# Kernel optimization log

Measured on AMD Instinct MI355X. Metric: run time of the kernel, lower is better.

Reference implementation:

```python
import jax, jax.numpy as jnp
import numpy as np

K = 6
EPS = 1e-7
BN_EPS = 1e-5


def tagconv(x, row, col, n, lins, bias, mw1, mb1, bng, bnb, mw2, mb2):
    # gcn_norm: symmetric normalization, no self-loops, edge_weight = 1
    deg = jax.ops.segment_sum(jnp.ones(row.shape[0], x.dtype), col, num_segments=n)
    dis = jnp.where(deg > 0, jax.lax.rsqrt(jnp.maximum(deg, 1.0)), 0.0)
    norm = dis[row] * dis[col]  # [E]
    out = x @ lins[0]
    h = x
    for k in range(1, K + 1):
        # message: relu(edge_weight * x_j) + eps, then scatter-add to destination
        msg = jax.nn.relu(norm[:, None] * h[row]) + EPS  # [E, C]
        h = jax.ops.segment_sum(msg, col, num_segments=n)
        out = out + h @ lins[k]
    out = out + bias
    # MLP: Linear -> BatchNorm1d(eval: running mean 0, var 1) -> ReLU -> Dropout(eval) -> Linear
    z = out @ mw1 + mb1
    z = bng * (z * (1.0 / np.sqrt(1.0 + BN_EPS))) + bnb
    z = jax.nn.relu(z)
    return z @ mw2 + mb2


def setup_inputs() -> dict:
    key = jax.random.key(0)
    ks = jax.random.split(key, 8)
    N, E, F, H, C = 50000, 800000, 128, 128, 64
    s = 0.05
    return {
        "x": jax.random.normal(ks[0], (N, F), jnp.float32),
        "edge_index": jax.random.randint(ks[1], (2, E), 0, N, jnp.int64),
        "lins1": jax.random.normal(ks[2], (K + 1, F, H), jnp.float32) * s,
        "bias1": jnp.zeros((H,), jnp.float32),
        "m1w1": jax.random.normal(ks[3], (H, 2 * H), jnp.float32) * s,
        "m1b1": jnp.zeros((2 * H,), jnp.float32),
        "bn1g": jnp.ones((2 * H,), jnp.float32),
        "bn1b": jnp.zeros((2 * H,), jnp.float32),
        "m1w2": jax.random.normal(ks[4], (2 * H, H), jnp.float32) * s,
        "m1b2": jnp.zeros((H,), jnp.float32),
        "lins2": jax.random.normal(ks[5], (K + 1, H, C), jnp.float32) * s,
        "bias2": jnp.zeros((C,), jnp.float32),
        "m2w1": jax.random.normal(ks[6], (C, 2 * C), jnp.float32) * s,
        "m2b1": jnp.zeros((2 * C,), jnp.float32),
        "bn2g": jnp.ones((2 * C,), jnp.float32),
        "bn2b": jnp.zeros((2 * C,), jnp.float32),
        "m2w2": jax.random.normal(ks[7], (2 * C, C), jnp.float32) * s,
        "m2b2": jnp.zeros((C,), jnp.float32),
    }


def reference(x, edge_index, lins1, bias1, m1w1, m1b1, bn1g, bn1b, m1w2, m1b2,
              lins2, bias2, m2w1, m2b1, bn2g, bn2b, m2w2, m2b2):
    n = x.shape[0]
    row, col = edge_index[0], edge_index[1]
    h = tagconv(x, row, col, n, lins1, bias1, m1w1, m1b1, bn1g, bn1b, m1w2, m1b2)
    h = jax.nn.relu(h)  # dropout is identity in eval mode
    return tagconv(h, row, col, n, lins2, bias2, m2w1, m2b1, bn2g, bn2b, m2w2, m2b2)
```

## Files before the change

### kernel.cpp

```cpp
#include <hip/hip_runtime.h>
#include <hip/hip_bf16.h>


#define EPS_MSG 1e-7f
#define BNSCALE 0.9999950000374997f
#define LO_INV 0.0009765625f

typedef _Float16 half_t;
typedef _Float16 f16x8 __attribute__((ext_vector_type(8)));
typedef float f32x4 __attribute__((ext_vector_type(4)));

__device__ __forceinline__ void gld16(const char* g, char* l) {
    __builtin_amdgcn_global_load_lds(
        (const __attribute__((address_space(1))) void*)g,
        (__attribute__((address_space(3))) void*)l, 16, 0, 0);
}

__device__ __forceinline__ float hlo(unsigned p) {
    unsigned short u = (unsigned short)(p & 0xffffu);
    half_t h;
    __builtin_memcpy(&h, &u, 2);
    return (float)h;
}
__device__ __forceinline__ float hhi(unsigned p) {
    unsigned short u = (unsigned short)(p >> 16);
    half_t h;
    __builtin_memcpy(&h, &u, 2);
    return (float)h;
}
__device__ __forceinline__ unsigned fpack2(float x, float y) {
    half_t a = (half_t)x, b = (half_t)y;
    unsigned short ua, ub;
    __builtin_memcpy(&ua, &a, 2);
    __builtin_memcpy(&ub, &b, 2);
    return (unsigned)ua | ((unsigned)ub << 16);
}


__global__ void zero_i32(int* __restrict__ p, int n) {
    int i = blockIdx.x * blockDim.x + threadIdx.x;
    if (i < n) p[i] = 0;
}

__global__ void count_deg(const int* __restrict__ col, int* __restrict__ deg, int E) {
    int e = blockIdx.x * blockDim.x + threadIdx.x;
    if (e < E) atomicAdd(&deg[col[e]], 1);
}

__global__ void compute_dis_s(const int* __restrict__ deg, float* __restrict__ dis,
                              float* __restrict__ s, float* __restrict__ rs, int N) {
    int v = blockIdx.x * blockDim.x + threadIdx.x;
    if (v >= N) return;
    int d = deg[v];
    float di = (d > 0) ? rsqrtf((float)d) : 0.f;
    dis[v] = di;
    s[v] = (d > 0) ? di : 1.f;
    rs[v] = (d > 0) ? sqrtf((float)d) : 1.f;
}

__global__ void scan_blk(const int* __restrict__ deg, int* __restrict__ off,
                         int* __restrict__ bsum, int N) {
    __shared__ int sm[1024];
    int i = blockIdx.x * 1024 + threadIdx.x;
    sm[threadIdx.x] = (i < N) ? deg[i] : 0;
    __syncthreads();
    for (int ofs = 1; ofs < 1024; ofs <<= 1) {
        int t = (threadIdx.x >= (unsigned)ofs) ? sm[threadIdx.x - ofs] : 0;
        __syncthreads();
        sm[threadIdx.x] += t;
        __syncthreads();
    }
    if (i < N) off[i + 1] = sm[threadIdx.x];
    if (threadIdx.x == 0) bsum[blockIdx.x] = sm[1023];
}

__global__ void scan_top(int* __restrict__ bsum, int nb) {
    if (threadIdx.x == 0 && blockIdx.x == 0) {
        int a = 0;
        for (int b = 0; b < nb; ++b) {
            int t = bsum[b];
            bsum[b] = a;
            a += t;
        }
    }
}

__global__ void scan_add(int* __restrict__ off, const int* __restrict__ bsum, int N) {
    int i = blockIdx.x * 1024 + threadIdx.x;
    if (i < N) off[i + 1] += bsum[blockIdx.x];
    if (i == 0) off[0] = 0;
}

__global__ void fill_edges(const int* __restrict__ row, const int* __restrict__ col,
                           const int* __restrict__ off, int* __restrict__ cur,
                           unsigned short* __restrict__ esrc, int E) {
    int e = blockIdx.x * blockDim.x + threadIdx.x;
    if (e >= E) return;
    int c = col[e];
    int pos = off[c] + atomicAdd(&cur[c], 1);
    esrc[pos] = (unsigned short)row[e];
}


__global__ void conv_xg(const float* __restrict__ x, half_t* __restrict__ slab,
                        half_t* __restrict__ g0, const float* __restrict__ dis,
                        const float* __restrict__ s, int total) {
    int i = blockIdx.x * blockDim.x + threadIdx.x;
    if (i >= total) return;
    int v = i >> 7, c = i & 127;
    float xv = x[i];
    slab[(size_t)v * 896 + c] = (half_t)(s[v] * xv);
    g0[i] = (half_t)(dis[v] * fmaxf(xv, 0.f));
}

__device__ __forceinline__ void wcv(const float* __restrict__ in, half_t* __restrict__ oh,
                                    half_t* __restrict__ ol, int nm, int K, int Nn, int i) {
    int KT = nm * K;
    int n = i / KT;
    int rem = i - n * KT;
    int km = rem / K, k = rem - km * K;
    float w = in[(size_t)km * K * Nn + (size_t)k * Nn + n];
    half_t h = (half_t)w;
    oh[i] = h;
    ol[i] = (half_t)((w - (float)h) * 1024.f);
}

__global__ void conv_all(const float* l1, const float* l2, const float* a1, const float* b1,
                         const float* a2, const float* b2, half_t* W1h, half_t* W1l,
                         half_t* W2h, half_t* W2l, half_t* M1ah, half_t* M1al, half_t* M1bh,
                         half_t* M1bl, half_t* M2ah, half_t* M2al, half_t* M2bh,
                         half_t* M2bl) {
    int i = blockIdx.x * blockDim.x + threadIdx.x;
    if (i < 114688) {
        wcv(l1, W1h, W1l, 7, 128, 128, i);
    } else if (i < 172032) {
        int j = i - 114688;
        int np = j >> 7, k = j & 127;
        int km = np >> 6, n = np & 63;
        float w = l2[(size_t)km * 128 * 64 + (size_t)k * 64 + n];
        half_t h = (half_t)w;
        W2h[j] = h;
        W2l[j] = (half_t)((w - (float)h) * 1024.f);
    } else if (i < 204800) {
        wcv(a1, M1ah, M1al, 1, 128, 256, i - 172032);
    } else if (i < 237568) {
        wcv(b1, M1bh, M1bl, 1, 256, 128, i - 204800);
    } else if (i < 245760) {
        wcv(a2, M2ah, M2al, 1, 64, 128, i - 237568);
    } else if (i < 253952) {
        wcv(b2, M2bh, M2bl, 1, 128, 64, i - 245760);
    }
}

__global__ void conv_trows(const float* __restrict__ l2, float* __restrict__ T) {
    __shared__ float sm[256];
    int j = blockIdx.x;
    int c = threadIdx.x & 63;
    int part = threadIdx.x >> 6;
    float a = 0.f;
    for (int k = j + 1; k <= 6; ++k)
        for (int kk = part; kk < 128; kk += 4)
            a += l2[(size_t)k * 128 * 64 + kk * 64 + c];
    sm[threadIdx.x] = a;
    __syncthreads();
    if (part == 0) T[j * 64 + c] = (sm[c] + sm[64 + c]) + (sm[128 + c] + sm[192 + c]);
}


__global__ void __launch_bounds__(256) prop(const unsigned* __restrict__ gin, int idl,
                                            unsigned* __restrict__ gout, int odl,
                                            const float* __restrict__ dis,
                                            const int* __restrict__ off,
                                            const unsigned short* __restrict__ esrc, int N) {
    const int lane = threadIdx.x & 63;
    const int w = threadIdx.x >> 6;
    const int stride = gridDim.x * 4;
    for (int v = blockIdx.x * 4 + w; v < N; v += stride) {
        int s = off[v], e = off[v + 1];
        float2 A0 = {0.f, 0.f}, A1 = {0.f, 0.f}, A2 = {0.f, 0.f}, A3 = {0.f, 0.f};
        float2 A4 = {0.f, 0.f}, A5 = {0.f, 0.f}, A6 = {0.f, 0.f}, A7 = {0.f, 0.f};
        for (int i = s; i < e; i += 8) {
            unsigned p[8];
            int ok[8];
#pragma unroll
            for (int j = 0; j < 8; ++j) {
                int ij = i + j;
                ok[j] = ij < e;
                int idx = ok[j] ? ij : e - 1;
                p[j] = gin[esrc[idx] * idl + lane];
            }
            A0.x += ok[0] ? hlo(p[0]) : 0.f; A0.y += ok[0] ? hhi(p[0]) : 0.f;
            A1.x += ok[1] ? hlo(p[1]) : 0.f; A1.y += ok[1] ? hhi(p[1]) : 0.f;
            A2.x += ok[2] ? hlo(p[2]) : 0.f; A2.y += ok[2] ? hhi(p[2]) : 0.f;
            A3.x += ok[3] ? hlo(p[3]) : 0.f; A3.y += ok[3] ? hhi(p[3]) : 0.f;
            A4.x += ok[4] ? hlo(p[4]) : 0.f; A4.y += ok[4] ? hhi(p[4]) : 0.f;
            A5.x += ok[5] ? hlo(p[5]) : 0.f; A5.y += ok[5] ? hhi(p[5]) : 0.f;
            A6.x += ok[6] ? hlo(p[6]) : 0.f; A6.y += ok[6] ? hhi(p[6]) : 0.f;
            A7.x += ok[7] ? hlo(p[7]) : 0.f; A7.y += ok[7] ? hhi(p[7]) : 0.f;
        }
        float ax = ((A0.x + A1.x) + (A2.x + A3.x)) + ((A4.x + A5.x) + (A6.x + A7.x));
        float ay = ((A0.y + A1.y) + (A2.y + A3.y)) + ((A4.y + A5.y) + (A6.y + A7.y));
        float dv = dis[v];
        float ce = (float)(e - s) * EPS_MSG;
        float hx = fmaf(dv, ax, ce);
        float hy = fmaf(dv, ay, ce);
        gout[v * odl + lane] = fpack2(dv * hx, dv * hy);
    }
}


template <int FINAL>
__global__ void __launch_bounds__(256) prop64(
    const half_t* __restrict__ uin, int ldu, const half_t* __restrict__ pj, int ldp,
    half_t* __restrict__ uout, int ldo, const float* __restrict__ dis,
    const int* __restrict__ off, const unsigned short* __restrict__ esrc,
    const float* __restrict__ tj, const float* __restrict__ bias2, int N) {
    const int c = threadIdx.x & 63;
    const int w = threadIdx.x >> 6;
    const int stride = gridDim.x * 4;
    for (int v = blockIdx.x * 4 + w; v < N; v += stride) {
        int s = off[v], e = off[v + 1];
        float a0 = 0.f, a1 = 0.f, a2 = 0.f, a3 = 0.f;
        float a4 = 0.f, a5 = 0.f, a6 = 0.f, a7 = 0.f;
        for (int i = s; i < e; i += 8) {
            float q[8];
            int ok[8];
#pragma unroll
            for (int j = 0; j < 8; ++j) {
                int ij = i + j;
                ok[j] = ij < e;
                int idx = ok[j] ? ij : e - 1;
                q[j] = (float)uin[(size_t)esrc[idx] * ldu + c];
            }
            a0 += ok[0] ? q[0] : 0.f;
            a1 += ok[1] ? q[1] : 0.f;
            a2 += ok[2] ? q[2] : 0.f;
            a3 += ok[3] ? q[3] : 0.f;
            a4 += ok[4] ? q[4] : 0.f;
            a5 += ok[5] ? q[5] : 0.f;
            a6 += ok[6] ? q[6] : 0.f;
            a7 += ok[7] ? q[7] : 0.f;
        }
        float acc = ((a0 + a1) + (a2 + a3)) + ((a4 + a5) + (a6 + a7));
        float dv = dis[v];
        float base = (float)pj[(size_t)v * ldp + c] + (float)(e - s) * EPS_MSG * tj[c];
        float u = fmaf(dv, acc, base);
        if (FINAL)
            uout[(size_t)v * ldo + c] = (half_t)(u + bias2[c]);
        else
            uout[(size_t)v * ldo + c] = (half_t)(dv * u);
    }
}


template <int OUTF32>
__global__ __launch_bounds__(256) void gemm(
    int M, int kiters, const half_t* __restrict__ A, int lda,
    const half_t* __restrict__ Bhp, const half_t* __restrict__ Blp, int ldb, int noff,
    void* __restrict__ Cp, int ldc, const float* __restrict__ rs, int epi,
    const float* __restrict__ bias, const float* __restrict__ bng,
    const float* __restrict__ bnb) {
    constexpr int BM = 64, BK = 64, BN = 64;
    constexpr int WROWS = 16;
    constexpr int NF = 4;
    constexpr int ABY = BM * BK * 2;
    constexpr int BBY = BN * BK * 2;
    constexpr int BUFBY = ABY + 2 * BBY;
    constexpr int ACW = 2, BCW = 2;

    __shared__ char lds[2][BUFBY];

    const int tid = threadIdx.x;
    const int lane = tid & 63;
    const int w = tid >> 6;
    const int m0 = blockIdx.x * BM;
    const int n0 = blockIdx.y * BN + noff;
    const int l15 = lane & 15, lq = lane >> 4;
    const int lr8 = lane >> 3, lc8 = lane & 7;

    const char* gA = (const char*)A;
    const char* gBh = (const char*)Bhp;
    const char* gBl = (const char*)Blp;
    const size_t ldaB = (size_t)lda * 2, ldbB = (size_t)ldb * 2;

    auto stage = [&](int kt, int buf) {
        const int k0b = kt * BK * 2;
        char* base = lds[0] + buf * BUFBY;
#pragma unroll
        for (int i = 0; i < ACW; ++i) {
            int c = w * ACW + i;
            int r = c * 8 + lr8;
            int gv = m0 + r;
            if (gv >= M) gv = M - 1;
            int sc = (lc8 ^ (r & 7)) << 4;
            gld16(gA + (size_t)gv * ldaB + k0b + sc, base + c * 1024);
        }
#pragma unroll
        for (int i = 0; i < BCW; ++i) {
            int c = w * BCW + i;
            int r = c * 8 + lr8;
            int sc = (lc8 ^ (r & 7)) << 4;
            size_t goff = (size_t)(n0 + r) * ldbB + k0b + sc;
            gld16(gBh + goff, base + ABY + c * 1024);
            gld16(gBl + goff, base + ABY + BBY + c * 1024);
        }
    };

    f32x4 acch[NF], accl[NF];
#pragma unroll
    for (int fn = 0; fn < NF; ++fn) {
        acch[fn] = (f32x4){0.f, 0.f, 0.f, 0.f};
        accl[fn] = (f32x4){0.f, 0.f, 0.f, 0.f};
    }

    auto compute = [&](int buf) {
        const char* Ab = lds[0] + buf * BUFBY;
        const char* Bhb = Ab + ABY;
        const char* Blb = Ab + ABY + BBY;
#pragma unroll
        for (int ks = 0; ks < 2; ++ks) {
            const int cc = ks * 4 + lq;
            int ra = w * WROWS + l15;
            f16x8 af = *(const f16x8*)(Ab + ra * 128 + ((cc ^ (ra & 7)) << 4));
#pragma unroll
            for (int fn = 0; fn < NF; ++fn) {
                int r = fn * 16 + l15;
                int o = r * 128 + ((cc ^ (r & 7)) << 4);
                f16x8 bhv = *(const f16x8*)(Bhb + o);
                f16x8 blv = *(const f16x8*)(Blb + o);
                acch[fn] = __builtin_amdgcn_mfma_f32_16x16x32_f16(af, bhv, acch[fn], 0, 0, 0);
                accl[fn] = __builtin_amdgcn_mfma_f32_16x16x32_f16(af, blv, accl[fn], 0, 0, 0);
            }
        }
    };

    stage(0, 0);
    int buf = 0;
    for (int kt = 0; kt < kiters; ++kt) {
        __syncthreads();
        if (kt + 1 < kiters) stage(kt + 1, buf ^ 1);
        compute(buf);
        buf ^= 1;
    }

#pragma unroll
    for (int fn = 0; fn < NF; ++fn)
#pragma unroll
        for (int i = 0; i < 4; ++i) {
            int gr = m0 + w * WROWS + (lane >> 4) * 4 + i;
            if (gr >= M) continue;
            int gc = n0 + fn * 16 + (lane & 15);
            float v = acch[fn][i] + accl[fn][i] * LO_INV;
            if (rs) v *= rs[gr];
            if (epi == 1) {
                v += bias[gc];
            } else if (epi == 2) {
                v = bng[gc] * ((v + bias[gc]) * BNSCALE) + bnb[gc];
                v = fmaxf(v, 0.f);
            } else if (epi == 3) {
                v = fmaxf(v + bias[gc], 0.f);
            }
            if (OUTF32)
                ((float*)Cp)[(size_t)gr * ldc + gc] = v;
            else
                ((half_t*)Cp)[(size_t)gr * ldc + gc] = (half_t)v;
        }
}

extern "C" void kernel_launch(void* const* d_in, const int* in_sizes, int n_in,
                              void* d_out, int out_size, void* d_ws, size_t ws_size,
                              hipStream_t stream) {
    const float* x     = (const float*)d_in[0];
    const int*   ei    = (const int*)d_in[1];
    const float* lins1 = (const float*)d_in[2];
    const float* bias1 = (const float*)d_in[3];
    const float* m1w1  = (const float*)d_in[4];
    const float* m1b1  = (const float*)d_in[5];
    const float* bn1g  = (const float*)d_in[6];
    const float* bn1b  = (const float*)d_in[7];
    const float* m1w2  = (const float*)d_in[8];
    const float* m1b2  = (const float*)d_in[9];
    const float* lins2 = (const float*)d_in[10];
    const float* bias2 = (const float*)d_in[11];
    const float* m2w1  = (const float*)d_in[12];
    const float* m2b1  = (const float*)d_in[13];
    const float* bn2g  = (const float*)d_in[14];
    const float* bn2b  = (const float*)d_in[15];
    const float* m2w2  = (const float*)d_in[16];
    const float* m2b2  = (const float*)d_in[17];
    float* out = (float*)d_out;

    const int N = in_sizes[0] / 128;
    const int E = in_sizes[1] / 2;
    const int* row = ei;
    const int* col = ei + E;

    char* ws = (char*)d_ws;
    size_t o = 0;
    auto alloc = [&](size_t bytes) {
        void* p = ws + o;
        o += (bytes + 255) & ~(size_t)255;
        return p;
    };
    int*            deg  = (int*)alloc((size_t)N * 4);
    int*            cur  = (int*)alloc((size_t)N * 4);
    float*          dis  = (float*)alloc((size_t)N * 4);
    float*          sA   = (float*)alloc((size_t)N * 4);
    float*          rsA  = (float*)alloc((size_t)N * 4);
    int*            off  = (int*)alloc((size_t)(N + 1) * 4);
    int*            bsum = (int*)alloc(1024 * 4);
    float*          Trow = (float*)alloc(6 * 64 * 4);
    unsigned short* esrc = (unsigned short*)alloc((size_t)E * 2);
    half_t* g0    = (half_t*)alloc((size_t)N * 128 * 2);
    half_t* ACC   = (half_t*)alloc((size_t)N * 128 * 2);
    half_t* Z     = (half_t*)alloc((size_t)N * 256 * 2);
    half_t* H1    = (half_t*)alloc((size_t)N * 128 * 2);
    half_t* ACC2  = (half_t*)alloc((size_t)N * 64 * 2);
    half_t* Wc1h  = (half_t*)alloc((size_t)128 * 896 * 2);
    half_t* Wc1l  = (half_t*)alloc((size_t)128 * 896 * 2);
    half_t* Wc2h  = (half_t*)alloc((size_t)448 * 128 * 2);
    half_t* Wc2l  = (half_t*)alloc((size_t)448 * 128 * 2);
    half_t* Wm1ah = (half_t*)alloc((size_t)256 * 128 * 2);
    half_t* Wm1al = (half_t*)alloc((size_t)256 * 128 * 2);
    half_t* Wm1bh = (half_t*)alloc((size_t)128 * 256 * 2);
    half_t* Wm1bl = (half_t*)alloc((size_t)128 * 256 * 2);
    half_t* Wm2ah = (half_t*)alloc((size_t)128 * 64 * 2);
    half_t* Wm2al = (half_t*)alloc((size_t)128 * 64 * 2);
    half_t* Wm2bh = (half_t*)alloc((size_t)64 * 128 * 2);
    half_t* Wm2bl = (half_t*)alloc((size_t)64 * 128 * 2);
    half_t* slab  = (half_t*)alloc((size_t)N * 896 * 2);
    (void)ws_size;

    const int TPB = 256;
    const int nb = (N + 1023) / 1024;
    zero_i32<<<(N + TPB - 1) / TPB, TPB, 0, stream>>>(deg, N);
    zero_i32<<<(N + TPB - 1) / TPB, TPB, 0, stream>>>(cur, N);
    count_deg<<<(E + TPB - 1) / TPB, TPB, 0, stream>>>(col, deg, E);
    compute_dis_s<<<(N + TPB - 1) / TPB, TPB, 0, stream>>>(deg, dis, sA, rsA, N);
    scan_blk<<<nb, 1024, 0, stream>>>(deg, off, bsum, N);
    scan_top<<<1, 64, 0, stream>>>(bsum, nb);
    scan_add<<<nb, 1024, 0, stream>>>(off, bsum, N);
    fill_edges<<<(E + TPB - 1) / TPB, TPB, 0, stream>>>(row, col, off, cur, esrc, E);
    conv_all<<<(253952 + TPB - 1) / TPB, TPB, 0, stream>>>(
        lins1, lins2, m1w1, m1w2, m2w1, m2w2, Wc1h, Wc1l, Wc2h, Wc2l, Wm1ah, Wm1al, Wm1bh,
        Wm1bl, Wm2ah, Wm2al, Wm2bh, Wm2bl);
    conv_trows<<<6, 256, 0, stream>>>(lins2, Trow);
    conv_xg<<<(N * 128 + TPB - 1) / TPB, TPB, 0, stream>>>(x, slab, g0, dis, sA, N * 128);

    unsigned* slabU = (unsigned*)slab;
    unsigned* g0U = (unsigned*)g0;
    const int HG = (N + 63) / 64;

    prop<<<2048, 256, 0, stream>>>(g0U, 64, slabU + 64, 448, dis, off, esrc, N);
    for (int k = 2; k <= 6; ++k)
        prop<<<2048, 256, 0, stream>>>(slabU + (size_t)(k - 1) * 64, 448,
                                       slabU + (size_t)k * 64, 448, dis, off, esrc, N);
    gemm<0><<<dim3(HG, 2), 256, 0, stream>>>(
        N, 14, slab, 896, Wc1h, Wc1l, 896, 0, ACC, 128, rsA, 1, bias1, nullptr, nullptr);
    gemm<0><<<dim3(HG, 4), 256, 0, stream>>>(
        N, 2, ACC, 128, Wm1ah, Wm1al, 128, 0, Z, 256, nullptr, 2, m1b1, bn1g, bn1b);
    gemm<0><<<dim3(HG, 2), 256, 0, stream>>>(
        N, 4, Z, 256, Wm1bh, Wm1bl, 256, 0, H1, 128, nullptr, 3, m1b2, nullptr, nullptr);

    gemm<0><<<dim3(HG, 6), 256, 0, stream>>>(
        N, 2, H1, 128, Wc2h, Wc2l, 128, 0, slab, 448, nullptr, 0, nullptr, nullptr, nullptr);
    gemm<0><<<dim3(HG, 1), 256, 0, stream>>>(
        N, 2, H1, 128, Wc2h, Wc2l, 128, 384, slab, 448, dis, 0, nullptr, nullptr, nullptr);

    half_t* ub0 = g0;
    half_t* ub1 = g0 + (size_t)N * 64;
    prop64<0><<<2048, 256, 0, stream>>>(slab + 384, 448, slab + 320, 448, ub0, 64, dis, off,
                                        esrc, Trow + 5 * 64, nullptr, N);
    prop64<0><<<2048, 256, 0, stream>>>(ub0, 64, slab + 256, 448, ub1, 64, dis, off, esrc,
                                        Trow + 4 * 64, nullptr, N);
    prop64<0><<<2048, 256, 0, stream>>>(ub1, 64, slab + 192, 448, ub0, 64, dis, off, esrc,
                                        Trow + 3 * 64, nullptr, N);
    prop64<0><<<2048, 256, 0, stream>>>(ub0, 64, slab + 128, 448, ub1, 64, dis, off, esrc,
                                        Trow + 2 * 64, nullptr, N);
    prop64<0><<<2048, 256, 0, stream>>>(ub1, 64, slab + 64, 448, ub0, 64, dis, off, esrc,
                                        Trow + 1 * 64, nullptr, N);
    prop64<1><<<2048, 256, 0, stream>>>(ub0, 64, slab, 448, ACC2, 64, dis, off, esrc,
                                        Trow + 0 * 64, bias2, N);

    gemm<0><<<dim3(HG, 2), 256, 0, stream>>>(
        N, 1, ACC2, 64, Wm2ah, Wm2al, 64, 0, Z, 128, nullptr, 2, m2b1, bn2g, bn2b);
    gemm<1><<<dim3(HG, 1), 256, 0, stream>>>(
        N, 2, Z, 128, Wm2bh, Wm2bl, 128, 0, out, 64, nullptr, 1, m2b2, nullptr, nullptr);
}
```

Before: 722.1 us.

## Load each A row tile once and loop over all output column strips

Replaces the 2D-grid GEMM, which re-read the A tile once per 64-wide column block, with two kernels. gemmc computes the full 128-wide output per block using a 2x2 wave layout with BK=32. gemmn keeps the whole 64xK A tile resident in LDS and streams B strips through it, double-buffered. It also merges the two separate lins2 GEMM launches into one, with a row scale applied to the last strip. The goal is to cut redundant global reads of A and launch count, at the cost of more LDS per block and serialised column strips within a block.

```diff
diff --git a/kernel.cpp b/kernel.cpp
--- a/kernel.cpp
+++ b/kernel.cpp
@@ -34,6 +34,21 @@
     __builtin_memcpy(&ua, &a, 2);
     __builtin_memcpy(&ub, &b, 2);
     return (unsigned)ua | ((unsigned)ub << 16);
+}
+
+__device__ __forceinline__ float epi_apply(float v, int gc, int epi,
+                                           const float* __restrict__ bias,
+                                           const float* __restrict__ bng,
+                                           const float* __restrict__ bnb) {
+    if (epi == 1) {
+        v += bias[gc];
+    } else if (epi == 2) {
+        v = bng[gc] * ((v + bias[gc]) * BNSCALE) + bnb[gc];
+        v = fmaxf(v, 0.f);
+    } else if (epi == 3) {
+        v = fmaxf(v + bias[gc], 0.f);
+    }
+    return v;
 }
 
 
@@ -253,30 +268,19 @@
 }
 
 
-template <int OUTF32>
-__global__ __launch_bounds__(256) void gemm(
+__global__ __launch_bounds__(256) void gemmc(
     int M, int kiters, const half_t* __restrict__ A, int lda,
-    const half_t* __restrict__ Bhp, const half_t* __restrict__ Blp, int ldb, int noff,
-    void* __restrict__ Cp, int ldc, const float* __restrict__ rs, int epi,
-    const float* __restrict__ bias, const float* __restrict__ bng,
-    const float* __restrict__ bnb) {
-    constexpr int BM = 64, BK = 64, BN = 64;
-    constexpr int WROWS = 16;
-    constexpr int NF = 4;
-    constexpr int ABY = BM * BK * 2;
-    constexpr int BBY = BN * BK * 2;
-    constexpr int BUFBY = ABY + 2 * BBY;
-    constexpr int ACW = 2, BCW = 2;
-
-    __shared__ char lds[2][BUFBY];
-
-    const int tid = threadIdx.x;
-    const int lane = tid & 63;
-    const int w = tid >> 6;
-    const int m0 = blockIdx.x * BM;
-    const int n0 = blockIdx.y * BN + noff;
+    const half_t* __restrict__ Bhp, const half_t* __restrict__ Blp, int ldb,
+    half_t* __restrict__ Cp, int ldc, const float* __restrict__ rs,
+    const float* __restrict__ bias) {
+    constexpr int ABY = 4096, BBY = 8192, BUFBY = ABY + 2 * BBY;
+    __shared__ __align__(16) char lds[2][BUFBY];
+
+    const int tid = threadIdx.x, lane = tid & 63, w = tid >> 6;
+    const int wr = w >> 1, wc = w & 1;
+    const int m0 = blockIdx.x * 64;
     const int l15 = lane & 15, lq = lane >> 4;
-    const int lr8 = lane >> 3, lc8 = lane & 7;
+    const int lr = lane >> 2, lc = lane & 3;
 
     const char* gA = (const char*)A;
     const char* gBh = (const char*)Bhp;
@@ -284,52 +288,55 @@
     const size_t ldaB = (size_t)lda * 2, ldbB = (size_t)ldb * 2;
 
     auto stage = [&](int kt, int buf) {
-        const int k0b = kt * BK * 2;
+        const int k0b = kt * 64;
         char* base = lds[0] + buf * BUFBY;
-#pragma unroll
-        for (int i = 0; i < ACW; ++i) {
-            int c = w * ACW + i;
-            int r = c * 8 + lr8;
+        {
+            int r = w * 16 + lr;
             int gv = m0 + r;
             if (gv >= M) gv = M - 1;
-            int sc = (lc8 ^ (r & 7)) << 4;
-            gld16(gA + (size_t)gv * ldaB + k0b + sc, base + c * 1024);
-        }
-#pragma unroll
-        for (int i = 0; i < BCW; ++i) {
-            int c = w * BCW + i;
-            int r = c * 8 + lr8;
-            int sc = (lc8 ^ (r & 7)) << 4;
-            size_t goff = (size_t)(n0 + r) * ldbB + k0b + sc;
+            int sc = (lc ^ (r & 3)) << 4;
+            gld16(gA + (size_t)gv * ldaB + k0b + sc, base + w * 1024);
+        }
+#pragma unroll
+        for (int i = 0; i < 2; ++i) {
+            int c = w * 2 + i;
+            int r = c * 16 + lr;
+            int sc = (lc ^ (r & 3)) << 4;
+            size_t goff = (size_t)r * ldbB + k0b + sc;
             gld16(gBh + goff, base + ABY + c * 1024);
             gld16(gBl + goff, base + ABY + BBY + c * 1024);
         }
     };
 
-    f32x4 acch[NF], accl[NF];
-#pragma unroll
-    for (int fn = 0; fn < NF; ++fn) {
-        acch[fn] = (f32x4){0.f, 0.f, 0.f, 0.f};
-        accl[fn] = (f32x4){0.f, 0.f, 0.f, 0.f};
-    }
+    f32x4 acch[2][4], accl[2][4];
+#pragma unroll
+    for (int fm = 0; fm < 2; ++fm)
+#pragma unroll
+        for (int fn = 0; fn < 4; ++fn) {
+            acch[fm][fn] = (f32x4){0.f, 0.f, 0.f, 0.f};
+            accl[fm][fn] = (f32x4){0.f, 0.f, 0.f, 0.f};
+        }
 
     auto compute = [&](int buf) {
         const char* Ab = lds[0] + buf * BUFBY;
         const char* Bhb = Ab + ABY;
         const char* Blb = Ab + ABY + BBY;
-#pragma unroll
-        for (int ks = 0; ks < 2; ++ks) {
-            const int cc = ks * 4 + lq;
-            int ra = w * WROWS + l15;
-            f16x8 af = *(const f16x8*)(Ab + ra * 128 + ((cc ^ (ra & 7)) << 4));
-#pragma unroll
-            for (int fn = 0; fn < NF; ++fn) {
-                int r = fn * 16 + l15;
-                int o = r * 128 + ((cc ^ (r & 7)) << 4);
-                f16x8 bhv = *(const f16x8*)(Bhb + o);
-                f16x8 blv = *(const f16x8*)(Blb + o);
-                acch[fn] = __builtin_amdgcn_mfma_f32_16x16x32_f16(af, bhv, acch[fn], 0, 0, 0);
-                accl[fn] = __builtin_amdgcn_mfma_f32_16x16x32_f16(af, blv, accl[fn], 0, 0, 0);
+        f16x8 af[2];
+#pragma unroll
+        for (int fm = 0; fm < 2; ++fm) {
+            int ra = wr * 32 + fm * 16 + l15;
+            af[fm] = *(const f16x8*)(Ab + ra * 64 + ((lq ^ (ra & 3)) << 4));
+        }
+#pragma unroll
+        for (int fn = 0; fn < 4; ++fn) {
+            int rb = wc * 64 + fn * 16 + l15;
+            int o = rb * 64 + ((lq ^ (rb & 3)) << 4);
+            f16x8 bhv = *(const f16x8*)(Bhb + o);
+            f16x8 blv = *(const f16x8*)(Blb + o);
+#pragma unroll
+            for (int fm = 0; fm < 2; ++fm) {
+                acch[fm][fn] = __builtin_amdgcn_mfma_f32_16x16x32_f16(af[fm], bhv, acch[fm][fn], 0, 0, 0);
+                accl[fm][fn] = __builtin_amdgcn_mfma_f32_16x16x32_f16(af[fm], blv, accl[fm][fn], 0, 0, 0);
             }
         }
     };
@@ -344,27 +351,125 @@
     }
 
 #pragma unroll
-    for (int fn = 0; fn < NF; ++fn)
-#pragma unroll
-        for (int i = 0; i < 4; ++i) {
-            int gr = m0 + w * WROWS + (lane >> 4) * 4 + i;
-            if (gr >= M) continue;
-            int gc = n0 + fn * 16 + (lane & 15);
-            float v = acch[fn][i] + accl[fn][i] * LO_INV;
-            if (rs) v *= rs[gr];
-            if (epi == 1) {
-                v += bias[gc];
-            } else if (epi == 2) {
-                v = bng[gc] * ((v + bias[gc]) * BNSCALE) + bnb[gc];
-                v = fmaxf(v, 0.f);
-            } else if (epi == 3) {
-                v = fmaxf(v + bias[gc], 0.f);
+    for (int fm = 0; fm < 2; ++fm)
+#pragma unroll
+        for (int fn = 0; fn < 4; ++fn)
+#pragma unroll
+            for (int i = 0; i < 4; ++i) {
+                int gr = m0 + wr * 32 + fm * 16 + lq * 4 + i;
+                if (gr >= M) continue;
+                int gc = wc * 64 + fn * 16 + l15;
+                float v = acch[fm][fn][i] + accl[fm][fn][i] * LO_INV;
+                v = v * rs[gr] + bias[gc];
+                Cp[(size_t)gr * ldc + gc] = (half_t)v;
             }
-            if (OUTF32)
-                ((float*)Cp)[(size_t)gr * ldc + gc] = v;
-            else
-                ((half_t*)Cp)[(size_t)gr * ldc + gc] = (half_t)v;
-        }
+}
+
+
+template <int KT, int NS, int OUTF32>
+__global__ __launch_bounds__(256) void gemmn(
+    int M, const half_t* __restrict__ A, int lda, const half_t* __restrict__ Bhp,
+    const half_t* __restrict__ Blp, int ldb, void* __restrict__ Cp, int ldc, int epi,
+    const float* __restrict__ bias, const float* __restrict__ bng,
+    const float* __restrict__ bnb, const float* __restrict__ scaleRows, int scaleStrip) {
+    constexpr int KI = KT / 32;
+    constexpr int T = NS * KI;
+    constexpr int CPR = KT / 8;
+    constexpr int LPR = CPR;
+    constexpr int RPC = 64 / LPR;
+    constexpr int SW = (CPR < 16) ? CPR - 1 : 15;
+    constexpr int ACH = (64 * KT * 2) / 1024;
+    constexpr int ACW = ACH / 4;
+    constexpr int ABY = 64 * KT * 2;
+    constexpr int BPB = 4096;
+    __shared__ __align__(16) char lds[ABY + 4 * BPB];
+
+    const int tid = threadIdx.x, lane = tid & 63, w = tid >> 6;
+    const int m0 = blockIdx.x * 64;
+    const int l15 = lane & 15, lq = lane >> 4;
+    const int lr = lane >> 2, lc = lane & 3;
+
+    const char* gA = (const char*)A;
+    const char* gBh = (const char*)Bhp;
+    const char* gBl = (const char*)Blp;
+    const size_t ldaB = (size_t)lda * 2, ldbB = (size_t)ldb * 2;
+
+#pragma unroll
+    for (int i = 0; i < ACW; ++i) {
+        int c = w * ACW + i;
+        int r = c * RPC + lane / LPR;
+        int col = lane % LPR;
+        int scol = col ^ (r & SW);
+        int gv = m0 + r;
+        if (gv >= M) gv = M - 1;
+        gld16(gA + (size_t)gv * ldaB + scol * 16, lds + c * 1024);
+    }
+
+    auto stageB = [&](int ns, int kt, int buf) {
+        char* bb = lds + ABY + buf * 2 * BPB;
+        int r = w * 16 + lr;
+        int sc = (lc ^ (r & 3)) << 4;
+        size_t goff = (size_t)(ns * 64 + r) * ldbB + kt * 64 + sc;
+        gld16(gBh + goff, bb + w * 1024);
+        gld16(gBl + goff, bb + BPB + w * 1024);
+    };
+
+    f32x4 acch[4], accl[4];
+
+    auto compute = [&](int buf, int kt) {
+        const char* Ab = lds;
+        const char* Bhb = lds + ABY + buf * 2 * BPB;
+        const char* Blb = Bhb + BPB;
+        int ra = w * 16 + l15;
+        int cc = kt * 4 + lq;
+        f16x8 af = *(const f16x8*)(Ab + ra * (KT * 2) + ((cc ^ (ra & SW)) << 4));
+#pragma unroll
+        for (int fn = 0; fn < 4; ++fn) {
+            int rb = fn * 16 + l15;
+            int o = rb * 64 + ((lq ^ (rb & 3)) << 4);
+            f16x8 bhv = *(const f16x8*)(Bhb + o);
+            f16x8 blv = *(const f16x8*)(Blb + o);
+            acch[fn] = __builtin_amdgcn_mfma_f32_16x16x32_f16(af, bhv, acch[fn], 0, 0, 0);
+            accl[fn] = __builtin_amdgcn_mfma_f32_16x16x32_f16(af, blv, accl[fn], 0, 0, 0);
+        }
+    };
+
+    stageB(0, 0, 0);
+    int buf = 0;
+    for (int t = 0; t < T; ++t) {
+        int ns = t / KI, kt = t - ns * KI;
+        __syncthreads();
+        if (t + 1 < T) {
+            int t1 = t + 1;
+            stageB(t1 / KI, t1 - (t1 / KI) * KI, buf ^ 1);
+        }
+        if (kt == 0) {
+#pragma unroll
+            for (int fn = 0; fn < 4; ++fn) {
+                acch[fn] = (f32x4){0.f, 0.f, 0.f, 0.f};
+                accl[fn] = (f32x4){0.f, 0.f, 0.f, 0.f};
+            }
+        }
+        compute(buf, kt);
+        if (kt == KI - 1) {
+#pragma unroll
+            for (int fn = 0; fn < 4; ++fn)
+#pragma unroll
+                for (int i = 0; i < 4; ++i) {
+                    int gr = m0 + w * 16 + lq * 4 + i;
+                    if (gr >= M) continue;
+                    int gc = ns * 64 + fn * 16 + l15;
+                    float v = acch[fn][i] + accl[fn][i] * LO_INV;
+                    if (ns == scaleStrip) v *= scaleRows[gr];
+                    v = epi_apply(v, gc, epi, bias, bng, bnb);
+                    if (OUTF32)
+                        ((float*)Cp)[(size_t)gr * ldc + gc] = v;
+                    else
+                        ((half_t*)Cp)[(size_t)gr * ldc + gc] = (half_t)v;
+                }
+        }
+        buf ^= 1;
+    }
 }
 
 extern "C" void kernel_launch(void* const* d_in, const int* in_sizes, int n_in,
@@ -455,17 +560,14 @@
     for (int k = 2; k <= 6; ++k)
         prop<<<2048, 256, 0, stream>>>(slabU + (size_t)(k - 1) * 64, 448,
                                        slabU + (size_t)k * 64, 448, dis, off, esrc, N);
-    gemm<0><<<dim3(HG, 2), 256, 0, stream>>>(
-        N, 14, slab, 896, Wc1h, Wc1l, 896, 0, ACC, 128, rsA, 1, bias1, nullptr, nullptr);
-    gemm<0><<<dim3(HG, 4), 256, 0, stream>>>(
-        N, 2, ACC, 128, Wm1ah, Wm1al, 128, 0, Z, 256, nullptr, 2, m1b1, bn1g, bn1b);
-    gemm<0><<<dim3(HG, 2), 256, 0, stream>>>(
-        N, 4, Z, 256, Wm1bh, Wm1bl, 256, 0, H1, 128, nullptr, 3, m1b2, nullptr, nullptr);
-
-    gemm<0><<<dim3(HG, 6), 256, 0, stream>>>(
-        N, 2, H1, 128, Wc2h, Wc2l, 128, 0, slab, 448, nullptr, 0, nullptr, nullptr, nullptr);
-    gemm<0><<<dim3(HG, 1), 256, 0, stream>>>(
-        N, 2, H1, 128, Wc2h, Wc2l, 128, 384, slab, 448, dis, 0, nullptr, nullptr, nullptr);
+    gemmc<<<HG, 256, 0, stream>>>(N, 28, slab, 896, Wc1h, Wc1l, 896, ACC, 128, rsA, bias1);
+    gemmn<128, 4, 0><<<HG, 256, 0, stream>>>(
+        N, ACC, 128, Wm1ah, Wm1al, 128, Z, 256, 2, m1b1, bn1g, bn1b, nullptr, -1);
+    gemmn<256, 2, 0><<<HG, 256, 0, stream>>>(
+        N, Z, 256, Wm1bh, Wm1bl, 256, H1, 128, 3, m1b2, nullptr, nullptr, nullptr, -1);
+
+    gemmn<128, 7, 0><<<HG, 256, 0, stream>>>(
+        N, H1, 128, Wc2h, Wc2l, 128, slab, 448, 0, nullptr, nullptr, nullptr, dis, 6);
 
     half_t* ub0 = g0;
     half_t* ub1 = g0 + (size_t)N * 64;
@@ -482,8 +584,8 @@
     prop64<1><<<2048, 256, 0, stream>>>(ub0, 64, slab, 448, ACC2, 64, dis, off, esrc,
                                         Trow + 0 * 64, bias2, N);
 
-    gemm<0><<<dim3(HG, 2), 256, 0, stream>>>(
-        N, 1, ACC2, 64, Wm2ah, Wm2al, 64, 0, Z, 128, nullptr, 2, m2b1, bn2g, bn2b);
-    gemm<1><<<dim3(HG, 1), 256, 0, stream>>>(
-        N, 2, Z, 128, Wm2bh, Wm2bl, 128, 0, out, 64, nullptr, 1, m2b2, nullptr, nullptr);
-}
+    gemmn<64, 2, 0><<<HG, 256, 0, stream>>>(
+        N, ACC2, 64, Wm2ah, Wm2al, 64, Z, 128, 2, m2b1, bn2g, bn2b, nullptr, -1);
+    gemmn<128, 1, 1><<<HG, 256, 0, stream>>>(
+        N, Z, 128, Wm2bh, Wm2bl, 128, out, 64, 1, m2b2, nullptr, nullptr, nullptr, -1);
+}
```

After: 675.6 us. 1.07x faster.
